# Optimization experiments

Hardware: AMD Instinct MI355X
Metric: run time of the kernel (lower is better)

The kernel has to match this reference:

```python
import jax, jax.numpy as jnp
import numpy as np

# Clos factorization for in=out=4096, middle_switch_multiplier=4:
BIN, B1, B2, B3, BOUT = 64, 64, 256, 64, 64
B, C, D = 2, 4096, 4096


def setup_inputs() -> dict:
    key = jax.random.key(0)
    ks = jax.random.split(key, 7)
    k = 1.0 / np.sqrt(D)
    x = jax.random.normal(ks[0], (B, C, D), dtype=jnp.float32)
    # kaiming_uniform(a=sqrt(5)) on [bin,b1,b2]-like tensors ~ uniform(-bound, bound)
    w1 = jax.random.uniform(ks[1], (BIN, B1, B2), jnp.float32, -k, k)
    w2 = jax.random.uniform(ks[2], (B1, B2, B3), jnp.float32, -k, k)
    w3 = jax.random.uniform(ks[3], (B2, B3, BOUT), jnp.float32, -k, k)
    bias1 = jax.random.uniform(ks[4], (B1,), jnp.float32, -k, k)
    bias2 = jax.random.uniform(ks[5], (B2,), jnp.float32, -k, k)
    bias3 = jax.random.uniform(ks[6], (B3,), jnp.float32, -k, k)
    return {"x": x, "w1": w1, "w2": w2, "w3": w3,
            "bias1": bias1, "bias2": bias2, "bias3": bias3}


def reference(x, w1, w2, w3, bias1, bias2, bias3):
    b, c, _ = x.shape
    h = x.reshape(b, c, BIN, B1)                      # [b,c,n=bin,r=b1]
    h = jnp.einsum('bcnr,nrm->bcmr', h, w1) + bias1   # [b,c,b2,b1] + bias over b1
    h = jnp.einsum('bcmr,rmn->bcnm', h, w2) + bias2   # [b,c,b3,b2] + bias over b2
    h = jnp.einsum('bcnm,mro->bcor', h, w3) + bias3   # [b,c,bout,b3] + bias over b3
    return h.reshape(b, c, -1)                        # [b,c,out_features]
```

## Files before the change

kernel.cpp:

```cpp
#include <hip/hip_runtime.h>
#include <stdint.h>
#include <stddef.h>

typedef __bf16 bf16_t;
typedef __bf16 bf16x8 __attribute__((ext_vector_type(8)));
typedef __bf16 bf16x4 __attribute__((ext_vector_type(4)));
typedef float f32x4 __attribute__((ext_vector_type(4)));

__device__ __forceinline__ void gload_lds16(const void* g, void* l) {
  __builtin_amdgcn_global_load_lds(
      (const __attribute__((address_space(1))) uint32_t*)g,
      (__attribute__((address_space(3))) uint32_t*)l, 16, 0, 0);
}

__global__ void prep1_k(const float* __restrict__ w2, const float* __restrict__ w3,
                        float* __restrict__ w2s, bf16_t* __restrict__ w3pt) {
  __shared__ float lds[64][65];
  const int b = blockIdx.x;
  const int t = threadIdx.x;
  if (b < 64) {
    const int r = b, m = t;
    const float4* p = (const float4*)(w2 + ((size_t)(r * 256 + m)) * 64);
    float s = 0.f;
#pragma unroll
    for (int i = 0; i < 16; ++i) {
      float4 v = p[i];
      s += (v.x + v.y) + (v.z + v.w);
    }
    w2s[r * 256 + m] = s;
    return;
  }
  const int b2 = b - 64;
  const int r = b2 & 63;
  const int mt = (b2 >> 6) * 64;
#pragma unroll
  for (int it = 0; it < 16; ++it) {
    int idx = t + it * 256;
    int ml = idx >> 6, o = idx & 63;
    lds[ml][o] = w3[(size_t)(mt + ml) * 4096 + r * 64 + o];
  }
  __syncthreads();
#pragma unroll
  for (int it = 0; it < 16; ++it) {
    int idx = t + it * 256;
    int o = idx >> 6, ml = idx & 63;
    w3pt[(size_t)(o * 64 + r) * 256 + mt + ml] = (bf16_t)lds[ml][o];
  }
}

__global__ void prep2_k(const float* __restrict__ w1, const float* __restrict__ w2s,
                        const float* __restrict__ bias1, const float* __restrict__ bias2,
                        bf16_t* __restrict__ w1t, float* __restrict__ c2) {
  __shared__ float lds[64][65];
  const int b = blockIdx.x;
  const int t = threadIdx.x;
  if (b == 256) {
    float s = 64.f * bias2[t];
#pragma unroll 8
    for (int r = 0; r < 64; ++r) s += bias1[r] * w2s[r * 256 + t];
    c2[t] = s;
    return;
  }
  const int k0 = (b >> 2) * 64;
  const int mt = (b & 3) * 64;
#pragma unroll
  for (int it = 0; it < 16; ++it) {
    int idx = t + it * 256;
    int kl = idx >> 6, ml = idx & 63;
    int k = k0 + kl;
    lds[kl][ml] = w1[(size_t)k * 256 + mt + ml] * w2s[(k & 63) * 256 + mt + ml];
  }
  __syncthreads();
#pragma unroll
  for (int it = 0; it < 16; ++it) {
    int idx = t + it * 256;
    int ml = idx >> 6, kl = idx & 63;
    w1t[(size_t)(mt + ml) * 4096 + k0 + kl] = (bf16_t)lds[kl][ml];
  }
}

__global__ __launch_bounds__(512, 4) void gemm1_k(
    const float* __restrict__ X, const bf16_t* __restrict__ W1T,
    bf16_t* __restrict__ S4) {
  __shared__ __align__(16) bf16_t lA[2][64 * 64];
  __shared__ __align__(16) bf16_t lB[2][256 * 64];
  const int tid = threadIdx.x;
  const int lane = tid & 63;
  const int wv = tid >> 6;
  const int mtile = (int)blockIdx.x >> 2;
  const int kh = (int)blockIdx.x & 3;
  const size_t m0 = (size_t)mtile * 64;
  const int kbase = kh * 1024;
  const int wm = wv >> 2, wn = wv & 3;
  const int r0 = tid >> 4;
  const int f4 = tid & 15;

  f32x4 acc[2][4];
#pragma unroll
  for (int i = 0; i < 2; ++i)
#pragma unroll
    for (int j = 0; j < 4; ++j) acc[i][j] = (f32x4){0.f, 0.f, 0.f, 0.f};

  float4 aR0[2], aR1[2];

  auto issueA = [&](float4 (&dst)[2], int kt) {
#pragma unroll
    for (int p = 0; p < 2; ++p) {
      int row = r0 + p * 32;
      dst[p] = *(const float4*)(X + (m0 + row) * 4096 + (size_t)(kbase + kt * 64 + f4 * 4));
    }
  };
  auto writeA = [&](const float4 (&src)[2], int buf) {
#pragma unroll
    for (int p = 0; p < 2; ++p) {
      int row = r0 + p * 32;
      int off = row * 128 + ((f4 * 8) ^ ((row & 7) << 4));
      bf16x4 v;
      v[0] = (bf16_t)src[p].x;
      v[1] = (bf16_t)src[p].y;
      v[2] = (bf16_t)src[p].z;
      v[3] = (bf16_t)src[p].w;
      *(bf16x4*)((char*)(&lA[buf][0]) + off) = v;
    }
  };
  auto issueB = [&](int buf, int kt) {
#pragma unroll
    for (int i = 0; i < 4; ++i) {
      int row = wv * 32 + i * 8 + (lane >> 3);
      int srckb = ((lane & 7) * 16) ^ ((row & 7) << 4);
      const char* src = (const char*)W1T + (size_t)row * 8192 + (size_t)(kbase + kt * 64) * 2 + srckb;
      char* dst = (char*)(&lB[buf][0]) + (wv * 32 + i * 8) * 128;
      gload_lds16(src, dst);
    }
  };
  auto compute = [&](int buf) {
#pragma unroll
    for (int kk = 0; kk < 2; ++kk) {
      const int kb = kk * 64 + ((lane >> 4) * 16);
      bf16x8 af[2], bfr[4];
#pragma unroll
      for (int mf = 0; mf < 2; ++mf) {
        int row = wm * 32 + mf * 16 + (lane & 15);
        int off = row * 128 + (kb ^ ((row & 7) << 4));
        af[mf] = *(const bf16x8*)((const char*)(&lA[buf][0]) + off);
      }
#pragma unroll
      for (int nf = 0; nf < 4; ++nf) {
        int row = wn * 64 + nf * 16 + (lane & 15);
        int off = row * 128 + (kb ^ ((row & 7) << 4));
        bfr[nf] = *(const bf16x8*)((const char*)(&lB[buf][0]) + off);
      }
#pragma unroll
      for (int mf = 0; mf < 2; ++mf)
#pragma unroll
        for (int nf = 0; nf < 4; ++nf)
          acc[mf][nf] = __builtin_amdgcn_mfma_f32_16x16x32_bf16(af[mf], bfr[nf], acc[mf][nf], 0, 0, 0);
    }
  };

  issueA(aR0, 0);
  issueB(0, 0);
  writeA(aR0, 0);
  issueA(aR1, 1);
  __syncthreads();
#pragma unroll 1
  for (int kt2 = 0; kt2 < 16; kt2 += 2) {
    if (kt2 + 1 < 16) issueB(1, kt2 + 1);
    compute(0);
    if (kt2 + 1 < 16) writeA(aR1, 1);
    if (kt2 + 2 < 16) issueA(aR0, kt2 + 2);
    __syncthreads();
    if (kt2 + 2 < 16) issueB(0, kt2 + 2);
    compute(1);
    if (kt2 + 2 < 16) writeA(aR0, 0);
    if (kt2 + 3 < 16) issueA(aR1, kt2 + 3);
    __syncthreads();
  }

#pragma unroll
  for (int nf = 0; nf < 4; ++nf) {
    int col = wn * 64 + nf * 16 + (lane & 15);
#pragma unroll
    for (int mf = 0; mf < 2; ++mf) {
#pragma unroll
      for (int q = 0; q < 4; ++q) {
        int row = wm * 32 + mf * 16 + (lane >> 4) * 4 + q;
        S4[(m0 + row) * 1024 + (size_t)(kh * 256 + col)] = (bf16_t)acc[mf][nf][q];
      }
    }
  }
}

__global__ __launch_bounds__(256) void reduce_k(
    const bf16_t* __restrict__ S4, const float* __restrict__ c2,
    bf16_t* __restrict__ S) {
  int gid = blockIdx.x * 256 + threadIdx.x;
  int row = gid >> 5;
  int c8 = (gid & 31) << 3;
  float s[8];
  float4 ca = *(const float4*)(c2 + c8);
  float4 cb = *(const float4*)(c2 + c8 + 4);
  s[0] = ca.x; s[1] = ca.y; s[2] = ca.z; s[3] = ca.w;
  s[4] = cb.x; s[5] = cb.y; s[6] = cb.z; s[7] = cb.w;
#pragma unroll
  for (int h = 0; h < 4; ++h) {
    bf16x8 v = *(const bf16x8*)(S4 + (size_t)row * 1024 + h * 256 + c8);
#pragma unroll
    for (int j = 0; j < 8; ++j) s[j] += (float)v[j];
  }
  bf16x8 o;
#pragma unroll
  for (int j = 0; j < 8; ++j) o[j] = (bf16_t)s[j];
  *(bf16x8*)(S + (size_t)row * 256 + c8) = o;
}

__global__ __launch_bounds__(512, 4) void gemm2_k(
    const bf16_t* __restrict__ S, const bf16_t* __restrict__ W3pT,
    const float* __restrict__ bias3, float* __restrict__ OUT) {
  __shared__ __align__(16) bf16_t lA[2][128 * 64];
  __shared__ __align__(16) bf16_t lB[2][128 * 64];
  const int tid = threadIdx.x;
  const int lane = tid & 63;
  const int wv = tid >> 6;
  const int bid = (int)blockIdx.x;
  const int newbid = (bid & 7) * 256 + (bid >> 3);
  const int mt = newbid >> 5;
  const int nt = newbid & 31;
  const size_t m0 = (size_t)mt * 128;
  const int n0 = nt * 128;
  const int wm = wv >> 2, wn = wv & 3;

  f32x4 acc[4][2];
#pragma unroll
  for (int i = 0; i < 4; ++i)
#pragma unroll
    for (int j = 0; j < 2; ++j) acc[i][j] = (f32x4){0.f, 0.f, 0.f, 0.f};

  auto stage = [&](int buf, int kt) {
#pragma unroll
    for (int p = 0; p < 2; ++p) {
      int row = wv * 8 + (lane >> 3) + p * 64;
      int srckb = ((lane & 7) * 16) ^ ((row & 7) << 4);
      const char* srcA = (const char*)S + (m0 + row) * 512 + (size_t)(kt * 128 + srckb);
      char* dstA = (char*)(&lA[buf][0]) + (wv * 8 + p * 64) * 128;
      gload_lds16(srcA, dstA);
      const char* srcB = (const char*)W3pT + (size_t)(n0 + row) * 512 + (size_t)(kt * 128 + srckb);
      char* dstB = (char*)(&lB[buf][0]) + (wv * 8 + p * 64) * 128;
      gload_lds16(srcB, dstB);
    }
  };
  auto compute = [&](int buf) {
#pragma unroll
    for (int kk = 0; kk < 2; ++kk) {
      const int kb = kk * 64 + ((lane >> 4) * 16);
      bf16x8 af[4], bfr[2];
#pragma unroll
      for (int mf = 0; mf < 4; ++mf) {
        int row = wm * 64 + mf * 16 + (lane & 15);
        int off = row * 128 + (kb ^ ((row & 7) << 4));
        af[mf] = *(const bf16x8*)((const char*)(&lA[buf][0]) + off);
      }
#pragma unroll
      for (int nf = 0; nf < 2; ++nf) {
        int row = wn * 32 + nf * 16 + (lane & 15);
        int off = row * 128 + (kb ^ ((row & 7) << 4));
        bfr[nf] = *(const bf16x8*)((const char*)(&lB[buf][0]) + off);
      }
#pragma unroll
      for (int mf = 0; mf < 4; ++mf)
#pragma unroll
        for (int nf = 0; nf < 2; ++nf)
          acc[mf][nf] = __builtin_amdgcn_mfma_f32_16x16x32_bf16(af[mf], bfr[nf], acc[mf][nf], 0, 0, 0);
    }
  };

  stage(0, 0);
  __syncthreads();
#pragma unroll 1
  for (int kt = 0; kt < 4; ++kt) {
    int cur = kt & 1;
    if (kt + 1 < 4) stage(cur ^ 1, kt + 1);
    compute(cur);
    __syncthreads();
  }

#pragma unroll
  for (int nf = 0; nf < 2; ++nf) {
    int jcol = wn * 32 + nf * 16 + (lane & 15);
    float b3 = bias3[jcol & 63];
    int j = n0 + jcol;
#pragma unroll
    for (int mf = 0; mf < 4; ++mf) {
#pragma unroll
      for (int q = 0; q < 4; ++q) {
        size_t row = m0 + (size_t)(wm * 64 + mf * 16 + (lane >> 4) * 4 + q);
        OUT[row * 4096 + j] = acc[mf][nf][q] + b3;
      }
    }
  }
}

extern "C" void kernel_launch(void* const* d_in, const int* in_sizes, int n_in,
                              void* d_out, int out_size, void* d_ws, size_t ws_size,
                              hipStream_t stream) {
  (void)in_sizes; (void)n_in; (void)out_size; (void)ws_size;
  const float* x  = (const float*)d_in[0];
  const float* w1 = (const float*)d_in[1];
  const float* w2 = (const float*)d_in[2];
  const float* w3 = (const float*)d_in[3];
  const float* b1 = (const float*)d_in[4];
  const float* b2 = (const float*)d_in[5];
  const float* b3 = (const float*)d_in[6];
  float* out = (float*)d_out;
  char* ws = (char*)d_ws;

  float*  w2s  = (float*)(ws + 0);
  float*  c2   = (float*)(ws + 65536);
  bf16_t* w1t  = (bf16_t*)(ws + 69632);
  bf16_t* w3pt = (bf16_t*)(ws + 69632 + 2097152);
  bf16_t* S4   = (bf16_t*)(ws + 69632 + 2 * 2097152);
  bf16_t* S    = (bf16_t*)(ws + 69632 + 2 * 2097152 + 16777216);

  prep1_k<<<320, 256, 0, stream>>>(w2, w3, w2s, w3pt);
  prep2_k<<<257, 256, 0, stream>>>(w1, w2s, b1, b2, w1t, c2);
  gemm1_k<<<512, 512, 0, stream>>>(x, w1t, S4);
  reduce_k<<<1024, 256, 0, stream>>>(S4, c2, S);
  gemm2_k<<<2048, 512, 0, stream>>>(S, w3pt, b3, out);
}
```

Baseline: 106.0 us.

## Replace syncthreads with fine-grained vmcnt waits and remap blocks to XCDs

Replaces __syncthreads in gemm1 and gemm2 with explicit s_waitcnt vmcnt/lgkmcnt plus raw s_barrier. This lets outstanding global loads stay in flight across iterations instead of draining everything at each barrier. The gemm1 loop is restructured with a peeled tail and reordered issue/write/compute. Block indices in gemm1, reduce and gemm2 are remapped so that blocks sharing the same rows land on the same XCD for L2 locality. Hand-counted vmcnt values are fragile: a miscount can cause races or stale LDS reads.

```diff
diff --git a/kernel.cpp b/kernel.cpp
--- a/kernel.cpp
+++ b/kernel.cpp
@@ -6,6 +6,15 @@
 typedef __bf16 bf16x8 __attribute__((ext_vector_type(8)));
 typedef __bf16 bf16x4 __attribute__((ext_vector_type(4)));
 typedef float f32x4 __attribute__((ext_vector_type(4)));
+
+#define VMW(n) asm volatile("s_waitcnt vmcnt(" #n ")" ::: "memory")
+#define LGKM0 asm volatile("s_waitcnt lgkmcnt(0)" ::: "memory")
+#define CFENCE asm volatile("" ::: "memory")
+#define RAWBAR              \
+  do {                      \
+    __builtin_amdgcn_s_barrier(); \
+    CFENCE;                 \
+  } while (0)
 
 __device__ __forceinline__ void gload_lds16(const void* g, void* l) {
   __builtin_amdgcn_global_load_lds(
@@ -87,8 +96,11 @@
   const int tid = threadIdx.x;
   const int lane = tid & 63;
   const int wv = tid >> 6;
-  const int mtile = (int)blockIdx.x >> 2;
-  const int kh = (int)blockIdx.x & 3;
+  const int bid = (int)blockIdx.x;
+  const int xcd = bid & 7;
+  const int rr = bid >> 3;
+  const int mtile = xcd * 16 + (rr >> 2);
+  const int kh = rr & 3;
   const size_t m0 = (size_t)mtile * 64;
   const int kbase = kh * 1024;
   const int wm = wv >> 2, wn = wv & 3;
@@ -101,7 +113,7 @@
 #pragma unroll
     for (int j = 0; j < 4; ++j) acc[i][j] = (f32x4){0.f, 0.f, 0.f, 0.f};
 
-  float4 aR0[2], aR1[2];
+  float4 s0[2], s1[2];
 
   auto issueA = [&](float4 (&dst)[2], int kt) {
 #pragma unroll
@@ -158,24 +170,50 @@
     }
   };
 
-  issueA(aR0, 0);
+  issueA(s0, 0);
+  CFENCE;
   issueB(0, 0);
-  writeA(aR0, 0);
-  issueA(aR1, 1);
-  __syncthreads();
+  CFENCE;
+  issueA(s1, 1);
+  CFENCE;
+  VMW(6);
+  writeA(s0, 0);
+  VMW(2);
+  LGKM0;
+  RAWBAR;
+
 #pragma unroll 1
-  for (int kt2 = 0; kt2 < 16; kt2 += 2) {
-    if (kt2 + 1 < 16) issueB(1, kt2 + 1);
+  for (int kt2 = 0; kt2 < 14; kt2 += 2) {
+    issueB(1, kt2 + 1);
+    CFENCE;
+    issueA(s0, kt2 + 2);
+    CFENCE;
+    VMW(6);
+    writeA(s1, 1);
     compute(0);
-    if (kt2 + 1 < 16) writeA(aR1, 1);
-    if (kt2 + 2 < 16) issueA(aR0, kt2 + 2);
-    __syncthreads();
-    if (kt2 + 2 < 16) issueB(0, kt2 + 2);
+    VMW(2);
+    LGKM0;
+    RAWBAR;
+    issueB(0, kt2 + 2);
+    CFENCE;
+    issueA(s1, kt2 + 3);
+    CFENCE;
+    VMW(6);
+    writeA(s0, 0);
     compute(1);
-    if (kt2 + 2 < 16) writeA(aR0, 0);
-    if (kt2 + 3 < 16) issueA(aR1, kt2 + 3);
-    __syncthreads();
-  }
+    VMW(2);
+    LGKM0;
+    RAWBAR;
+  }
+  issueB(1, 15);
+  CFENCE;
+  VMW(4);
+  writeA(s1, 1);
+  compute(0);
+  VMW(0);
+  LGKM0;
+  RAWBAR;
+  compute(1);
 
 #pragma unroll
   for (int nf = 0; nf < 4; ++nf) {
@@ -194,9 +232,11 @@
 __global__ __launch_bounds__(256) void reduce_k(
     const bf16_t* __restrict__ S4, const float* __restrict__ c2,
     bf16_t* __restrict__ S) {
-  int gid = blockIdx.x * 256 + threadIdx.x;
-  int row = gid >> 5;
-  int c8 = (gid & 31) << 3;
+  const int bid = (int)blockIdx.x;
+  const int base = (bid & 7) * 1024 + (bid >> 3) * 8;
+  const int t = threadIdx.x;
+  const int row = base + (t >> 5);
+  const int c8 = (t & 31) << 3;
   float s[8];
   float4 ca = *(const float4*)(c2 + c8);
   float4 cb = *(const float4*)(c2 + c8 + 4);
@@ -223,9 +263,10 @@
   const int lane = tid & 63;
   const int wv = tid >> 6;
   const int bid = (int)blockIdx.x;
-  const int newbid = (bid & 7) * 256 + (bid >> 3);
-  const int mt = newbid >> 5;
-  const int nt = newbid & 31;
+  const int xcd = bid & 7;
+  const int rest = bid >> 3;
+  const int mt = xcd * 8 + (rest >> 5);
+  const int nt = rest & 31;
   const size_t m0 = (size_t)mt * 128;
   const int n0 = nt * 128;
   const int wm = wv >> 2, wn = wv & 3;
@@ -275,13 +316,21 @@
   };
 
   stage(0, 0);
-  __syncthreads();
+  CFENCE;
+  VMW(0);
+  RAWBAR;
 #pragma unroll 1
   for (int kt = 0; kt < 4; ++kt) {
     int cur = kt & 1;
-    if (kt + 1 < 4) stage(cur ^ 1, kt + 1);
+    if (kt + 1 < 4) {
+      stage(cur ^ 1, kt + 1);
+      CFENCE;
+    }
     compute(cur);
-    __syncthreads();
+    if (kt + 1 < 4) {
+      VMW(0);
+      RAWBAR;
+    }
   }
 
 #pragma unroll
```

After: 107.6 us. About the same (+1.4%).
